# Kernel tuning notes

Measured on AMD Instinct MI355X. Metric: run time of the kernel, lower is better.

## Reference

```python
import jax, jax.numpy as jnp
import numpy as np

D_MODEL = 1024
N_HEADS = 16
D_KEY = 64
EPS = 1e-5


def setup_inputs() -> dict:
    key = jax.random.key(0)
    ks = jax.random.split(key, 12)
    d, h, dk = D_MODEL, N_HEADS, D_KEY
    s = lambda fan_in: 1.0 / np.sqrt(fan_in)
    inp = {
        "X": jax.random.normal(ks[0], (2, 2048, d), dtype=jnp.float32),
        "Wqkv": jax.random.uniform(ks[1], (d, 3 * h * dk), jnp.float32, -s(d), s(d)),
        "bqkv": jax.random.uniform(ks[2], (3 * h * dk,), jnp.float32, -s(d), s(d)),
        "Wo": jax.random.uniform(ks[3], (h * dk, d), jnp.float32, -s(h * dk), s(h * dk)),
        "bo": jax.random.uniform(ks[4], (d,), jnp.float32, -s(h * dk), s(h * dk)),
        "W1": jax.random.uniform(ks[5], (d, 4 * d), jnp.float32, -s(d), s(d)),
        "b1": jax.random.uniform(ks[6], (4 * d,), jnp.float32, -s(d), s(d)),
        "W2": jax.random.uniform(ks[7], (4 * d, d), jnp.float32, -s(4 * d), s(4 * d)),
        "b2": jax.random.uniform(ks[8], (d,), jnp.float32, -s(4 * d), s(4 * d)),
        "ln1_g": jnp.ones((d,), jnp.float32),
        "ln1_b": jnp.zeros((d,), jnp.float32),
        "ln2_g": jnp.ones((d,), jnp.float32),
        "ln2_b": jnp.zeros((d,), jnp.float32),
    }
    return inp


def _layernorm(x, g, b):
    mu = jnp.mean(x, axis=-1, keepdims=True)
    var = jnp.var(x, axis=-1, keepdims=True)
    return (x - mu) * jax.lax.rsqrt(var + EPS) * g + b


def _block(X, Wqkv, bqkv, Wo, bo, W1, b1, W2, b2, ln1_g, ln1_b, ln2_g, ln2_b):
    B, T, _ = X.shape
    h, dk = N_HEADS, D_KEY
    # --- causal multi-head self-attention on LN(X) ---
    Xn = _layernorm(X, ln1_g, ln1_b)
    qkv = (Xn @ Wqkv + bqkv).reshape(B, T, 3, h, dk)
    q, k, v = (jnp.moveaxis(qkv, 2, 0)[i].transpose(0, 2, 1, 3) for i in range(3))  # each [B,h,T,dk]
    scores = jnp.einsum("bhqd,bhkd->bhqk", q, k) / np.sqrt(dk).astype(np.float32)
    causal = jnp.tril(jnp.ones((T, T), dtype=bool))
    scores = jnp.where(causal, scores, -jnp.inf)
    attn = jax.nn.softmax(scores, axis=-1)
    ctx = jnp.einsum("bhqk,bhkd->bhqd", attn, v)  # [B,h,T,dk]
    ctx = ctx.transpose(0, 2, 1, 3).reshape(B, T, h * dk)
    atten = ctx @ Wo + bo
    X = X + atten  # dropout is identity in eval mode
    # --- FFN on LN(X) ---
    Xn2 = _layernorm(X, ln2_g, ln2_b)
    ffn = jax.nn.relu(Xn2 @ W1 + b1) @ W2 + b2
    return X + ffn


def reference(X, Wqkv, bqkv, Wo, bo, W1, b1, W2, b2, ln1_g, ln1_b, ln2_g, ln2_b):
    return _block(X, Wqkv, bqkv, Wo, bo, W1, b1, W2, b2, ln1_g, ln1_b, ln2_g, ln2_b)
```

## Files before the change

kernel.cpp:

```cpp
#include <hip/hip_runtime.h>
#include <hip/hip_bf16.h>

typedef __hip_bfloat16 bf16;
typedef __attribute__((ext_vector_type(8))) short short8;
typedef __attribute__((ext_vector_type(4))) float f32x4;

constexpr int D     = 1024;
constexpr int T     = 2048;
constexpr int BATCH = 2;
constexpr int ROWS  = BATCH * T;
constexpr int NH    = 16;
constexpr int DKEY  = 64;
constexpr int QKVN  = 3 * D;
constexpr int FFNN  = 4 * D;

static __device__ __forceinline__ float b2f(bf16 x) { return __bfloat162float(x); }
static __device__ __forceinline__ bf16  f2b(float x) { return __float2bfloat16(x); }
static __device__ __forceinline__ float loadf(const bf16* p)  { return __bfloat162float(*p); }
static __device__ __forceinline__ float loadf(const float* p) { return *p; }
static __device__ __forceinline__ float fast_exp2(float x) { return __builtin_amdgcn_exp2f(x); }
static __device__ __forceinline__ unsigned short f2bu(float x) {
    return __bfloat16_as_ushort(__float2bfloat16(x));
}

static __device__ __forceinline__ void gload_lds16(const bf16* g, unsigned short* l) {
    __builtin_amdgcn_global_load_lds(
        (const __attribute__((address_space(1))) void*)g,
        (__attribute__((address_space(3))) void*)l,
        16, 0, 0);
}

__global__ __launch_bounds__(256) void transpose_cast(const float* __restrict__ in,
                                                      bf16* __restrict__ out,
                                                      int R, int C)
{
    __shared__ float tile[32][33];
    int c0 = blockIdx.x * 32, r0 = blockIdx.y * 32;
    int tx = threadIdx.x & 31, ty = threadIdx.x >> 5;
#pragma unroll
    for (int i = 0; i < 32; i += 8)
        tile[ty + i][tx] = in[(size_t)(r0 + ty + i) * C + c0 + tx];
    __syncthreads();
#pragma unroll
    for (int i = 0; i < 32; i += 8)
        out[(size_t)(c0 + ty + i) * R + r0 + tx] = f2b(tile[tx][ty + i]);
}

template <typename TIN>
__global__ __launch_bounds__(256) void ln_kernel(const TIN* __restrict__ X,
                                                 const float* __restrict__ g,
                                                 const float* __restrict__ b,
                                                 bf16* __restrict__ out)
{
    int row = blockIdx.x;
    int tid = threadIdx.x;
    const TIN* xr = X + (size_t)row * D;
    float v[4];
#pragma unroll
    for (int i = 0; i < 4; ++i) v[i] = loadf(xr + tid + i * 256);

    float s1 = v[0] + v[1] + v[2] + v[3];
    float s2 = v[0]*v[0] + v[1]*v[1] + v[2]*v[2] + v[3]*v[3];
#pragma unroll
    for (int off = 32; off; off >>= 1) {
        s1 += __shfl_xor(s1, off);
        s2 += __shfl_xor(s2, off);
    }
    __shared__ float red[8];
    int lane = tid & 63, w = tid >> 6;
    if (lane == 0) { red[w] = s1; red[4 + w] = s2; }
    __syncthreads();
    s1 = red[0] + red[1] + red[2] + red[3];
    s2 = red[4] + red[5] + red[6] + red[7];

    float mu   = s1 * (1.0f / D);
    float var  = s2 * (1.0f / D) - mu * mu;
    float rstd = rsqrtf(var + 1e-5f);

    bf16* orow = out + (size_t)row * D;
#pragma unroll
    for (int i = 0; i < 4; ++i) {
        int c = tid + i * 256;
        orow[c] = f2b((v[i] - mu) * rstd * g[c] + b[c]);
    }
}

template <int BM, int RELU, int RES, int OUTF32, int SPLITZ = 0>
__global__ __launch_bounds__(256) void mfma_gemm(
    const bf16* __restrict__ A, const bf16* __restrict__ Bt,
    const float* __restrict__ bias, const void* __restrict__ resid,
    void* __restrict__ out, float* __restrict__ part,
    int M, int N, int K, int Kstride)
{
    constexpr int MT = BM / 32;
    __shared__ __align__(16) unsigned short As[2][BM * 32];
    __shared__ __align__(16) unsigned short Bs[2][128 * 32];

    int gx = gridDim.x, gy = gridDim.y;
    int lid = (blockIdx.z * gy + blockIdx.y) * gx + blockIdx.x;
    int nwg = gx * gy * gridDim.z;
    int chunk = nwg >> 3;
    int swz = (lid & 7) * chunk + (lid >> 3);
    int bx = swz % gx;
    int by = (swz / gx) % gy;
    int bz = swz / (gx * gy);

    int tid  = threadIdx.x;
    int m0   = by * BM, n0 = bx * 128;
    int lane = tid & 63, wave = tid >> 6;
    int wm = (wave >> 1) * (MT * 16), wn = (wave & 1) * 64;
    int c15 = lane & 15, quad = lane >> 4;

    int koff = 0;
    if constexpr (SPLITZ) koff = bz * K;

    f32x4 acc[MT][4] = {};

    int srow = lane >> 2;
    int scol = (lane & 3) * 8;
    const bf16* abase = A  + (size_t)m0 * Kstride + koff;
    const bf16* bbase = Bt + (size_t)n0 * Kstride + koff;

    auto stage = [&](int buf, int kt) {
        int ko = kt * 32;
#pragma unroll
        for (int j = 0; j < 2; ++j) {
            int r = wave * 32 + j * 16;
            gload_lds16(bbase + (size_t)(r + srow) * Kstride + ko + scol,
                        &Bs[buf][r * 32]);
        }
        if constexpr (BM == 128) {
#pragma unroll
            for (int j = 0; j < 2; ++j) {
                int r = wave * 32 + j * 16;
                gload_lds16(abase + (size_t)(r + srow) * Kstride + ko + scol,
                            &As[buf][r * 32]);
            }
        } else {
            int r = wave * 16;
            gload_lds16(abase + (size_t)(r + srow) * Kstride + ko + scol,
                        &As[buf][r * 32]);
        }
    };

    int nk = K >> 5;
    stage(0, 0);
    __syncthreads();

    for (int kt = 0; kt < nk; ++kt) {
        int buf = kt & 1;
        if (kt + 1 < nk) stage(buf ^ 1, kt + 1);

        short8 af[MT], bfr[4];
#pragma unroll
        for (int t = 0; t < MT; ++t)
            af[t]  = *(const short8*)&As[buf][(wm + t * 16 + c15) * 32 + quad * 8];
#pragma unroll
        for (int t = 0; t < 4; ++t)
            bfr[t] = *(const short8*)&Bs[buf][(wn + t * 16 + c15) * 32 + quad * 8];
#pragma unroll
        for (int mt = 0; mt < MT; ++mt)
#pragma unroll
            for (int nt = 0; nt < 4; ++nt)
                acc[mt][nt] = __builtin_amdgcn_mfma_f32_16x16x32_bf16(
                    af[mt], bfr[nt], acc[mt][nt], 0, 0, 0);

        __syncthreads();
    }

#pragma unroll
    for (int mt = 0; mt < MT; ++mt) {
#pragma unroll
        for (int nt = 0; nt < 4; ++nt) {
            f32x4 v4 = acc[mt][nt];
            int gc = n0 + wn + nt * 16 + c15;
            float bb = (!SPLITZ || bz == 0) ? bias[gc] : 0.0f;
#pragma unroll
            for (int r = 0; r < 4; ++r) {
                int gr = m0 + wm + mt * 16 + quad * 4 + r;
                float v = v4[r] + bb;
                if constexpr (RELU) v = fmaxf(v, 0.0f);
                size_t idx = (size_t)gr * N + gc;
                if constexpr (SPLITZ) {
                    if (bz == 0) {
                        v += b2f(((const bf16*)resid)[idx]);
                        ((float*)out)[idx] = v;
                    } else {
                        part[idx] = v;
                    }
                } else {
                    if constexpr (RES == 1) v += b2f(((const bf16*)resid)[idx]);
                    if constexpr (RES == 2) v += ((const float*)resid)[idx];
                    if constexpr (OUTF32) ((float*)out)[idx] = v;
                    else                  ((bf16*)out)[idx] = f2b(v);
                }
            }
        }
    }
}

__global__ __launch_bounds__(256) void add_partial(float* __restrict__ out,
                                                   const float* __restrict__ part)
{
    int i = blockIdx.x * 256 + threadIdx.x;
    f32x4 a = ((const f32x4*)out)[i];
    f32x4 p = ((const f32x4*)part)[i];
    a += p;
    ((f32x4*)out)[i] = a;
}

__global__ __launch_bounds__(256) void flash_attn(const bf16* __restrict__ qkv,
                                                  bf16* __restrict__ ctx)
{
    constexpr int KROW = 72;
    constexpr float CSC = 0.18033688011112042f;
    constexpr float MSH = 12.0f;

    __shared__ __align__(16) unsigned short Qs[64 * KROW];
    __shared__ __align__(16) unsigned short Ks[64 * KROW];
    __shared__ __align__(16) unsigned short Vt[64 * KROW];
    unsigned short* Pt = Qs;

    int bx = blockIdx.x;
    int bh = bx & 31;
    int qi = 31 - (bx >> 5);
    int h  = bh & 15, b = bh >> 4;
    int q0 = qi * 64;

    int tid = threadIdx.x, lane = tid & 63, w = tid >> 6;
    int c15 = lane & 15, quad = lane >> 4;

    const bf16* base = qkv + (size_t)b * T * QKVN;

    {
        int row = tid >> 2, qtr = tid & 3;
        const bf16* src = base + (size_t)(q0 + row) * QKVN + h * 64 + qtr * 16;
        unsigned short* dst = &Qs[row * KROW + qtr * 16];
        uint4 v0 = *(const uint4*)(src);
        uint4 v1 = *(const uint4*)(src + 8);
        *(uint4*)(dst)     = v0;
        *(uint4*)(dst + 8) = v1;
    }
    __syncthreads();

    short8 qf[2];
#pragma unroll
    for (int s = 0; s < 2; ++s)
        qf[s] = *(const short8*)&Qs[(w * 16 + c15) * KROW + s * 32 + quad * 8];

    short8 ones;
#pragma unroll
    for (int i = 0; i < 8; ++i) ones[i] = (short)0x3F80;

    f32x4 Ot[4] = {};
    f32x4 lacc  = {};

    int nkt   = q0 / 64 + 1;
    int wqmin = q0 + w * 16;

    for (int kt = 0; kt < nkt; ++kt) {
        int k0 = kt * 64;
        int key = tid >> 2, seg = tid & 3;
        const bf16* ksrc = base + (size_t)(k0 + key) * QKVN + D + h * 64 + seg * 16;
        uint4 kv0 = *(const uint4*)ksrc;
        uint4 kv1 = *(const uint4*)(ksrc + 8);
        int keyp = (tid & 31) * 2, dk0 = (tid >> 5) * 8;
        const bf16* vsrc = base + (size_t)(k0 + keyp) * QKVN + 2 * D + h * 64 + dk0;
        uint4 vv0 = *(const uint4*)vsrc;
        uint4 vv1 = *(const uint4*)(vsrc + QKVN);

        __syncthreads();
        {
            unsigned short* kd = &Ks[key * KROW + seg * 16];
            *(uint4*)kd       = kv0;
            *(uint4*)(kd + 8) = kv1;
            const unsigned short* lo = (const unsigned short*)&vv0;
            const unsigned short* hi = (const unsigned short*)&vv1;
#pragma unroll
            for (int j = 0; j < 8; ++j) {
                unsigned int pk = (unsigned int)lo[j] | ((unsigned int)hi[j] << 16);
                *(unsigned int*)&Vt[(dk0 + j) * KROW + keyp] = pk;
            }
        }
        __syncthreads();

        f32x4 St[4] = {};
#pragma unroll
        for (int s = 0; s < 2; ++s)
#pragma unroll
            for (int ktm = 0; ktm < 4; ++ktm) {
                short8 kf = *(const short8*)&Ks[(ktm * 16 + c15) * KROW + s * 32 + quad * 8];
                St[ktm] = __builtin_amdgcn_mfma_f32_16x16x32_bf16(kf, qf[s], St[ktm], 0, 0, 0);
            }

        if (kt == nkt - 1) {
            int q_g = wqmin + c15;
#pragma unroll
            for (int ktm = 0; ktm < 4; ++ktm) {
                ushort4 pk;
#pragma unroll
                for (int r = 0; r < 4; ++r) {
                    float p = fast_exp2(fmaf(St[ktm][r], CSC, -MSH));
                    if (k0 + ktm * 16 + quad * 4 + r > q_g) p = 0.0f;
                    ((unsigned short*)&pk)[r] = f2bu(p);
                }
                *(ushort4*)&Pt[(w * 16 + c15) * KROW + ktm * 16 + quad * 4] = pk;
            }
        } else {
#pragma unroll
            for (int ktm = 0; ktm < 4; ++ktm) {
                ushort4 pk;
#pragma unroll
                for (int r = 0; r < 4; ++r)
                    ((unsigned short*)&pk)[r] = f2bu(fast_exp2(fmaf(St[ktm][r], CSC, -MSH)));
                *(ushort4*)&Pt[(w * 16 + c15) * KROW + ktm * 16 + quad * 4] = pk;
            }
        }

#pragma unroll
        for (int s = 0; s < 2; ++s) {
            short8 pf = *(const short8*)&Pt[(w * 16 + c15) * KROW + s * 32 + quad * 8];
            lacc = __builtin_amdgcn_mfma_f32_16x16x32_bf16(ones, pf, lacc, 0, 0, 0);
#pragma unroll
            for (int dt = 0; dt < 4; ++dt) {
                short8 vf = *(const short8*)&Vt[(dt * 16 + c15) * KROW + s * 32 + quad * 8];
                Ot[dt] = __builtin_amdgcn_mfma_f32_16x16x32_bf16(vf, pf, Ot[dt], 0, 0, 0);
            }
        }
    }

    {
        float inv = 1.0f / lacc[0];
        int grow = b * T + q0 + w * 16 + c15;
        bf16* dst = ctx + (size_t)grow * D + h * 64 + quad * 4;
#pragma unroll
        for (int dt = 0; dt < 4; ++dt) {
            ushort4 pk;
#pragma unroll
            for (int r = 0; r < 4; ++r)
                ((unsigned short*)&pk)[r] = f2bu(Ot[dt][r] * inv);
            *(ushort4*)(dst + dt * 16) = pk;
        }
    }
}

extern "C" void kernel_launch(void* const* d_in, const int* in_sizes, int n_in,
                              void* d_out, int out_size, void* d_ws, size_t ws_size,
                              hipStream_t stream)
{
    const float* X    = (const float*)d_in[0];
    const float* Wqkv = (const float*)d_in[1];
    const float* bqkv = (const float*)d_in[2];
    const float* Wo   = (const float*)d_in[3];
    const float* bo   = (const float*)d_in[4];
    const float* W1   = (const float*)d_in[5];
    const float* b1   = (const float*)d_in[6];
    const float* W2   = (const float*)d_in[7];
    const float* b2   = (const float*)d_in[8];
    const float* ln1g = (const float*)d_in[9];
    const float* ln1b = (const float*)d_in[10];
    const float* ln2g = (const float*)d_in[11];
    const float* ln2b = (const float*)d_in[12];
    float* out = (float*)d_out;

    char* ws = (char*)d_ws;
    bf16* Wqkv_t = (bf16*)(ws + 0);
    bf16* Wo_t   = (bf16*)(ws + 6291456);
    bf16* W1_t   = (bf16*)(ws + 8388608);
    bf16* W2_t   = (bf16*)(ws + 16777216);
    bf16* Xn     = (bf16*)(ws + 25165824);
    bf16* X1     = Xn;
    bf16* qkv    = (bf16*)(ws + 33554432);
    bf16* Xn2    = (bf16*)(ws + 33554432);
    bf16* ctx    = (bf16*)(ws + 58720256);
    bf16* mid    = (bf16*)(ws + 41943040);
    float* W2part = (float*)(ws + 0);

    transpose_cast<<<dim3(QKVN / 32, D / 32), 256, 0, stream>>>(Wqkv, Wqkv_t, D, QKVN);
    transpose_cast<<<dim3(D / 32, D / 32), 256, 0, stream>>>(Wo, Wo_t, D, D);
    transpose_cast<<<dim3(FFNN / 32, D / 32), 256, 0, stream>>>(W1, W1_t, D, FFNN);
    transpose_cast<<<dim3(D / 32, FFNN / 32), 256, 0, stream>>>(W2, W2_t, FFNN, D);

    ln_kernel<float><<<ROWS, 256, 0, stream>>>(X, ln1g, ln1b, Xn);
    mfma_gemm<128, 0, 0, 0><<<dim3(QKVN / 128, ROWS / 128), 256, 0, stream>>>(
        Xn, Wqkv_t, bqkv, nullptr, qkv, nullptr, ROWS, QKVN, D, D);
    flash_attn<<<1024, 256, 0, stream>>>(qkv, ctx);
    mfma_gemm<64, 0, 2, 0><<<dim3(D / 128, ROWS / 64), 256, 0, stream>>>(
        ctx, Wo_t, bo, X, X1, nullptr, ROWS, D, D, D);
    ln_kernel<bf16><<<ROWS, 256, 0, stream>>>(X1, ln2g, ln2b, Xn2);
    mfma_gemm<128, 1, 0, 0><<<dim3(FFNN / 128, ROWS / 128), 256, 0, stream>>>(
        Xn2, W1_t, b1, nullptr, mid, nullptr, ROWS, FFNN, D, D);
    mfma_gemm<64, 0, 1, 1, 1><<<dim3(D / 128, ROWS / 64, 2), 256, 0, stream>>>(
        mid, W2_t, b2, X1, out, W2part, ROWS, D, FFNN / 2, FFNN);
    add_partial<<<ROWS * D / 4 / 256, 256, 0, stream>>>(out, W2part);
}
```

Before: 347.0 us.

## Add triple-buffered LDS pipeline with one barrier per k-step to FFN GEMMs

```diff
diff --git a/kernel.cpp b/kernel.cpp
--- a/kernel.cpp
+++ b/kernel.cpp
@@ -85,7 +85,7 @@
     }
 }
 
-template <int BM, int RELU, int RES, int OUTF32, int SPLITZ = 0>
+template <int BM, int RELU, int RES, int OUTF32, int SPLITZ, int PIPE>
 __global__ __launch_bounds__(256) void mfma_gemm(
     const bf16* __restrict__ A, const bf16* __restrict__ Bt,
     const float* __restrict__ bias, const void* __restrict__ resid,
@@ -93,8 +93,9 @@
     int M, int N, int K, int Kstride)
 {
     constexpr int MT = BM / 32;
-    __shared__ __align__(16) unsigned short As[2][BM * 32];
-    __shared__ __align__(16) unsigned short Bs[2][128 * 32];
+    constexpr int NB = PIPE ? 3 : 2;
+    __shared__ __align__(16) unsigned short As[NB][BM * 32];
+    __shared__ __align__(16) unsigned short Bs[NB][128 * 32];
 
     int gx = gridDim.x, gy = gridDim.y;
     int lid = (blockIdx.z * gy + blockIdx.y) * gx + blockIdx.x;
@@ -143,14 +144,7 @@
         }
     };
 
-    int nk = K >> 5;
-    stage(0, 0);
-    __syncthreads();
-
-    for (int kt = 0; kt < nk; ++kt) {
-        int buf = kt & 1;
-        if (kt + 1 < nk) stage(buf ^ 1, kt + 1);
-
+    auto compute = [&](int buf) {
         short8 af[MT], bfr[4];
 #pragma unroll
         for (int t = 0; t < MT; ++t)
@@ -164,8 +158,40 @@
             for (int nt = 0; nt < 4; ++nt)
                 acc[mt][nt] = __builtin_amdgcn_mfma_f32_16x16x32_bf16(
                     af[mt], bfr[nt], acc[mt][nt], 0, 0, 0);
-
+    };
+
+    int nk = K >> 5;
+
+    if constexpr (PIPE == 0) {
+        stage(0, 0);
         __syncthreads();
+        for (int kt = 0; kt < nk; ++kt) {
+            int buf = kt & 1;
+            if (kt + 1 < nk) stage(buf ^ 1, kt + 1);
+            compute(buf);
+            __syncthreads();
+        }
+    } else {
+        stage(0, 0);
+        stage(1, 1);
+        int buf = 0, nbuf = 2;
+        for (int kt = 0; kt < nk; ++kt) {
+            if (kt + 1 < nk) {
+                if constexpr (BM == 128) asm volatile("s_waitcnt vmcnt(4)" ::: "memory");
+                else                     asm volatile("s_waitcnt vmcnt(3)" ::: "memory");
+            } else {
+                asm volatile("s_waitcnt vmcnt(0)" ::: "memory");
+            }
+            asm volatile("s_waitcnt lgkmcnt(0)" ::: "memory");
+            __builtin_amdgcn_s_barrier();
+            __builtin_amdgcn_sched_barrier(0);
+
+            if (kt + 2 < nk) stage(nbuf, kt + 2);
+            compute(buf);
+
+            buf  = (buf  == 2) ? 0 : buf  + 1;
+            nbuf = (nbuf == 2) ? 0 : nbuf + 1;
+        }
     }
 
 #pragma unroll
@@ -382,15 +408,15 @@
     transpose_cast<<<dim3(D / 32, FFNN / 32), 256, 0, stream>>>(W2, W2_t, FFNN, D);
 
     ln_kernel<float><<<ROWS, 256, 0, stream>>>(X, ln1g, ln1b, Xn);
-    mfma_gemm<128, 0, 0, 0><<<dim3(QKVN / 128, ROWS / 128), 256, 0, stream>>>(
+    mfma_gemm<128, 0, 0, 0, 0, 0><<<dim3(QKVN / 128, ROWS / 128), 256, 0, stream>>>(
         Xn, Wqkv_t, bqkv, nullptr, qkv, nullptr, ROWS, QKVN, D, D);
     flash_attn<<<1024, 256, 0, stream>>>(qkv, ctx);
-    mfma_gemm<64, 0, 2, 0><<<dim3(D / 128, ROWS / 64), 256, 0, stream>>>(
+    mfma_gemm<64, 0, 2, 0, 0, 0><<<dim3(D / 128, ROWS / 64), 256, 0, stream>>>(
         ctx, Wo_t, bo, X, X1, nullptr, ROWS, D, D, D);
     ln_kernel<bf16><<<ROWS, 256, 0, stream>>>(X1, ln2g, ln2b, Xn2);
-    mfma_gemm<128, 1, 0, 0><<<dim3(FFNN / 128, ROWS / 128), 256, 0, stream>>>(
+    mfma_gemm<128, 1, 0, 0, 0, 1><<<dim3(FFNN / 128, ROWS / 128), 256, 0, stream>>>(
         Xn2, W1_t, b1, nullptr, mid, nullptr, ROWS, FFNN, D, D);
-    mfma_gemm<64, 0, 1, 1, 1><<<dim3(D / 128, ROWS / 64, 2), 256, 0, stream>>>(
+    mfma_gemm<64, 0, 1, 1, 1, 1><<<dim3(D / 128, ROWS / 64, 2), 256, 0, stream>>>(
         mid, W2_t, b2, X1, out, W2part, ROWS, D, FFNN / 2, FFNN);
     add_partial<<<ROWS * D / 4 / 256, 256, 0, stream>>>(out, W2part);
 }
```

Measured after the change: 349.5 us. Within noise of the previous version (+0.7%).
